# Performance work log

Measured on AMD Instinct MI355X. Metric: run time of the kernel, lower is better.

The kernel has to match this reference:

```python
import jax, jax.numpy as jnp
import numpy as np

B, H, W = 8, 64, 64
DIM, NH, WS = 384, 6, 14
HD = DIM // NH
MLP = int(DIM * 4.0)
EPS = 1e-5
SCALE = HD ** -0.5


def setup_inputs() -> dict:
    key = jax.random.key(0)
    ks = jax.random.split(key, 8)
    init = lambda k, shape: (jax.random.normal(k, shape, dtype=jnp.float32) * 0.02)
    return {
        "x": jax.random.normal(ks[0], (B, H, W, DIM), dtype=jnp.float32),
        "ln1_w": jnp.ones((DIM,), jnp.float32),
        "ln1_b": jnp.zeros((DIM,), jnp.float32),
        "qkv_w": init(ks[1], (DIM, 3 * DIM)),
        "qkv_b": jnp.zeros((3 * DIM,), jnp.float32),
        "proj_w": init(ks[2], (DIM, DIM)),
        "proj_b": jnp.zeros((DIM,), jnp.float32),
        "rel_pos_h": init(ks[3], (2 * WS - 1, HD)),
        "rel_pos_w": init(ks[4], (2 * WS - 1, HD)),
        "ln2_w": jnp.ones((DIM,), jnp.float32),
        "ln2_b": jnp.zeros((DIM,), jnp.float32),
        "fc1_w": init(ks[5], (DIM, MLP)),
        "fc1_b": jnp.zeros((MLP,), jnp.float32),
        "fc2_w": init(ks[6], (MLP, DIM)),
        "fc2_b": jnp.zeros((DIM,), jnp.float32),
    }


def _layernorm(x, w, b):
    m = x.mean(-1, keepdims=True)
    v = ((x - m) ** 2).mean(-1, keepdims=True)
    return (x - m) * jax.lax.rsqrt(v + EPS) * w + b


def _get_rel_pos(rel_pos, ws):
    # q_size == k_size == ws and rel_pos has 2*ws-1 rows, so torch's
    # F.interpolate to max_rel_dist=2*ws-1 is an identity; direct indexing.
    coords = jnp.arange(ws)[:, None] - jnp.arange(ws)[None, :] + (ws - 1)
    return rel_pos[coords]  # (ws, ws, head_dim)


def _attention(xw, qkv_w, qkv_b, proj_w, proj_b, rel_pos_h, rel_pos_w):
    Bw = xw.shape[0]
    N = WS * WS
    qkv = xw.reshape(Bw, N, DIM) @ qkv_w + qkv_b  # (Bw, N, 3*DIM)
    qkv = qkv.reshape(Bw, N, 3, NH, HD).transpose(2, 0, 3, 1, 4).reshape(3, Bw * NH, N, HD)
    q, k, v = qkv[0], qkv[1], qkv[2]
    attn = jnp.einsum("bqd,bkd->bqk", q * SCALE, k)  # (Bw*NH, N, N)
    Rh = _get_rel_pos(rel_pos_h, WS)
    Rw = _get_rel_pos(rel_pos_w, WS)
    rq = q.reshape(Bw * NH, WS, WS, HD)
    rel_h = jnp.einsum("bhwc,hkc->bhwk", rq, Rh)
    rel_w = jnp.einsum("bhwc,wkc->bhwk", rq, Rw)
    attn = (attn.reshape(Bw * NH, WS, WS, WS, WS)
            + rel_h[:, :, :, :, None]
            + rel_w[:, :, :, None, :]).reshape(Bw * NH, N, N)
    attn = jax.nn.softmax(attn, axis=-1)
    out = jnp.einsum("bqk,bkd->bqd", attn, v)
    out = out.reshape(Bw, NH, WS, WS, HD).transpose(0, 2, 3, 1, 4).reshape(Bw, WS, WS, DIM)
    return out @ proj_w + proj_b


def reference(x, ln1_w, ln1_b, qkv_w, qkv_b, proj_w, proj_b, rel_pos_h, rel_pos_w,
              ln2_w, ln2_b, fc1_w, fc1_b, fc2_w, fc2_b):
    shortcut = x
    h = _layernorm(x, ln1_w, ln1_b)
    pad_h = (WS - H % WS) % WS
    pad_w = (WS - W % WS) % WS
    Hp, Wp = H + pad_h, W + pad_w
    hp = jnp.pad(h, ((0, 0), (0, pad_h), (0, pad_w), (0, 0)))
    # window partition: (B, Hp, Wp, C) -> (B*nWin, WS, WS, C)
    wins = hp.reshape(B, Hp // WS, WS, Wp // WS, WS, DIM)
    wins = wins.transpose(0, 1, 3, 2, 4, 5).reshape(-1, WS, WS, DIM)
    wins = _attention(wins, qkv_w, qkv_b, proj_w, proj_b, rel_pos_h, rel_pos_w)
    # window unpartition
    y = wins.reshape(B, Hp // WS, Wp // WS, WS, WS, DIM)
    y = y.transpose(0, 1, 3, 2, 4, 5).reshape(B, Hp, Wp, DIM)[:, :H, :W, :]
    x = shortcut + y
    h2 = _layernorm(x, ln2_w, ln2_b)
    mlp = jax.nn.gelu(h2 @ fc1_w + fc1_b, approximate=False) @ fc2_w + fc2_b
    return x + mlp
```

## Files before the change

kernel.cpp:

```cpp
#include <hip/hip_runtime.h>
#include <math.h>

#define DIMC 384
#define NHD  6
#define HD   64
#define WSZ  14
#define NTOK 196
#define NWIN 200
#define NWH  1200
#define MWIN 39200
#define MX   32768
#define MLPD 1536

typedef short short8 __attribute__((ext_vector_type(8)));
typedef float f32x4 __attribute__((ext_vector_type(4)));
typedef float f32x16 __attribute__((ext_vector_type(16)));

__device__ __forceinline__ unsigned short f2bf(float f) {
  unsigned int u = __float_as_uint(f);
  u = (u + 0x7fffu + ((u >> 16) & 1u)) >> 16;
  return (unsigned short)u;
}
__device__ __forceinline__ unsigned int pkbf(float a, float b) {
  unsigned int r; asm("v_cvt_pk_bf16_f32 %0, %1, %2" : "=v"(r) : "v"(a), "v"(b)); return r;
}
__device__ __forceinline__ float gelu_t(float x) {
  float z = 1.5957691216057308f * (x + 0.044715f * x * x * x);
  float e = __expf(z);
  float th = 1.f - 2.f * __builtin_amdgcn_rcpf(e + 1.f);
  return 0.5f * x * (1.f + th);
}

typedef const __attribute__((address_space(1))) unsigned int* gptr_t;
typedef __attribute__((address_space(3))) unsigned int* lptr_t;
__device__ __forceinline__ void gload16(const unsigned short* g, unsigned short* l) {
  __builtin_amdgcn_global_load_lds((gptr_t)(const void*)g, (lptr_t)(void*)l, 16, 0, 0);
}

#define SEG0 442368
#define SEG1 589824
#define SEG2 1179648
#define SEG3 1769472
#define SEG4 1773568
#define SEG5 2003968
__global__ void prep_kernel(const float* __restrict__ qkvw, const float* __restrict__ projw,
                            const float* __restrict__ fc1w, const float* __restrict__ fc2w,
                            const float* __restrict__ relh, const float* __restrict__ relw,
                            unsigned short* __restrict__ qkvwT, unsigned short* __restrict__ projwT,
                            unsigned short* __restrict__ fc1wT, unsigned short* __restrict__ fc2wT,
                            unsigned short* __restrict__ relcat, unsigned short* __restrict__ vT) {
  int id = blockIdx.x * 256 + threadIdx.x;
  if (id < SEG0) {
    int n = id / 384, k = id - n * 384;
    qkvwT[id] = f2bf(qkvw[(size_t)k * 1152 + n]);
  } else if (id < SEG1) {
    id -= SEG0;
    int n = id / 384, k = id - n * 384;
    projwT[id] = f2bf(projw[(size_t)k * 384 + n]);
  } else if (id < SEG2) {
    id -= SEG1;
    int n = id / 384, k = id - n * 384;
    fc1wT[id] = f2bf(fc1w[(size_t)k * 1536 + n]);
  } else if (id < SEG3) {
    id -= SEG2;
    int n = id / 1536, k = id - n * 1536;
    fc2wT[id] = f2bf(fc2w[(size_t)k * 384 + n]);
  } else if (id < SEG4) {
    id -= SEG3;
    int rc = id >> 6, d = id & 63;
    float v = 0.f;
    if (rc < 27) v = relh[rc * 64 + d] * 8.f;
    else if (rc < 54) v = relw[(rc - 27) * 64 + d] * 8.f;
    relcat[id] = f2bf(v);
  } else if (id < SEG5) {
    id -= SEG4;
    int row = id / 3, part = id - row * 3;
    *(int2*)(vT + (size_t)row * 208 + 196 + part * 4) = make_int2(0, 0);
  }
}

__global__ __launch_bounds__(64) void ln1win_kernel(const float* __restrict__ x,
    const float* __restrict__ w, const float* __restrict__ b, unsigned short* __restrict__ xw) {
  int t = blockIdx.x;
  int lane = threadIdx.x;
  int win = t / NTOK, p = t - win * NTOK;
  int bb = win / 25, rem = win - bb * 25;
  int wi = rem / 5, wj = rem - wi * 5;
  int i = p / WSZ, j = p - i * WSZ;
  int r = wi * WSZ + i, c = wj * WSZ + j;
  unsigned short* o = xw + (size_t)t * DIMC;
  if (r >= 64 || c >= 64) {
    #pragma unroll
    for (int q = 0; q < 6; q++) o[lane + q * 64] = 0;
    return;
  }
  const float* xr = x + (((size_t)bb * 64 + r) * 64 + c) * DIMC;
  float v[6]; float s = 0.f, s2 = 0.f;
  #pragma unroll
  for (int q = 0; q < 6; q++) { float f = xr[lane + q * 64]; v[q] = f; s += f; s2 += f * f; }
  #pragma unroll
  for (int off = 32; off; off >>= 1) { s += __shfl_xor(s, off); s2 += __shfl_xor(s2, off); }
  float mean = s * (1.f / DIMC);
  float var  = s2 * (1.f / DIMC) - mean * mean;
  float rstd = rsqrtf(var + 1e-5f);
  #pragma unroll
  for (int q = 0; q < 6; q++) {
    int d = lane + q * 64;
    o[d] = f2bf((v[q] - mean) * rstd * w[d] + b[d]);
  }
}

__global__ __launch_bounds__(64) void ln2_kernel(const float* __restrict__ x2,
    const float* __restrict__ w, const float* __restrict__ b, unsigned short* __restrict__ h2) {
  int t = blockIdx.x; int lane = threadIdx.x;
  const float* xr = x2 + (size_t)t * DIMC;
  unsigned short* o = h2 + (size_t)t * DIMC;
  float v[6]; float s = 0.f, s2 = 0.f;
  #pragma unroll
  for (int q = 0; q < 6; q++) { float f = xr[lane + q * 64]; v[q] = f; s += f; s2 += f * f; }
  #pragma unroll
  for (int off = 32; off; off >>= 1) { s += __shfl_xor(s, off); s2 += __shfl_xor(s2, off); }
  float mean = s * (1.f / DIMC);
  float var  = s2 * (1.f / DIMC) - mean * mean;
  float rstd = rsqrtf(var + 1e-5f);
  #pragma unroll
  for (int q = 0; q < 6; q++) {
    int d = lane + q * 64;
    o[d] = f2bf((v[q] - mean) * rstd * w[d] + b[d]);
  }
}

template <int EPI>
__global__ __launch_bounds__(256) void gemm_kernel(
    const unsigned short* __restrict__ A, const unsigned short* __restrict__ WT,
    int Mrows, int Kd,
    const float* __restrict__ bias, const float* __restrict__ addin,
    float* __restrict__ outf, unsigned short* __restrict__ outb,
    unsigned short* __restrict__ outb2) {
  __shared__ unsigned short As[3][128 * 32];
  __shared__ unsigned short Bs[3][128 * 32];
  const int nwg = gridDim.x * gridDim.y;
  const int flat = blockIdx.y * gridDim.x + blockIdx.x;
  const int xcd = flat & 7, q_ = nwg >> 3, r_ = nwg & 7;
  const int wg = (xcd < r_ ? xcd * (q_ + 1) : r_ * (q_ + 1) + (xcd - r_) * q_) + (flat >> 3);
  const int bx = wg / gridDim.y, by = wg - bx * gridDim.y;
  const int row0 = bx * 128, col0 = by * 128;
  const int tid = threadIdx.x;
  const int l = tid & 63, wid = tid >> 6;
  const int fr = l & 15, fk = (l >> 4) * 8;
  const int wr = (wid >> 1) * 64, wc = (wid & 1) * 64;
  const int sr = l >> 2, sc = (l & 3) * 8;
  const int scs = sc ^ (((sr >> 1) & 3) << 3);
  const int rsw = ((fr >> 1) & 3) << 3;
  f32x4 acc[4][4] = {};
  const unsigned short* ap = A + (size_t)row0 * Kd;
  const unsigned short* bp = WT + (size_t)col0 * Kd;
  const int nt = Kd >> 5;

  auto stage = [&](int t, int b) {
    const int k0 = t * 32;
    #pragma unroll
    for (int j = 0; j < 2; j++) {
      int chunk = j * 4 + wid;
      gload16(ap + (size_t)(chunk * 16 + sr) * Kd + k0 + scs, &As[b][chunk * 512]);
      gload16(bp + (size_t)(chunk * 16 + sr) * Kd + k0 + scs, &Bs[b][chunk * 512]);
    }
  };
  stage(0, 0);
  stage(1, 1);
  int c = 0;
  for (int t = 0; t < nt; ++t) {
    if (t < nt - 1) asm volatile("s_waitcnt vmcnt(4)" ::: "memory");
    else            asm volatile("s_waitcnt vmcnt(0)" ::: "memory");
    __builtin_amdgcn_s_barrier();
    __builtin_amdgcn_sched_barrier(0);
    if (t + 2 < nt) stage(t + 2, (c + 2 >= 3) ? c - 1 : c + 2);
    short8 a[4], b[4];
    #pragma unroll
    for (int fi = 0; fi < 4; fi++) {
      a[fi] = *(const short8*)&As[c][(wr + fi * 16 + fr) * 32 + (fk ^ rsw)];
      b[fi] = *(const short8*)&Bs[c][(wc + fi * 16 + fr) * 32 + (fk ^ rsw)];
    }
    __builtin_amdgcn_s_setprio(1);
    #pragma unroll
    for (int fi = 0; fi < 4; fi++)
      #pragma unroll
      for (int fj = 0; fj < 4; fj++)
        acc[fi][fj] = __builtin_amdgcn_mfma_f32_16x16x32_bf16(b[fj], a[fi], acc[fi][fj], 0, 0, 0);
    __builtin_amdgcn_s_setprio(0);
    c = (c + 1 >= 3) ? 0 : c + 1;
  }
  #pragma unroll
  for (int fi = 0; fi < 4; fi++) {
    const int gr = row0 + wr + fi * 16 + fr;
    if (gr >= Mrows) continue;
    int wv_ = 0, p = 0, valid = 1; size_t pixbase = 0;
    if (EPI == 0 || EPI == 1) { wv_ = gr / NTOK; p = gr - wv_ * NTOK; }
    if (EPI == 1) {
      int bb = wv_ / 25, rem2 = wv_ - bb * 25;
      int wi = rem2 / 5, wj = rem2 - wi * 5;
      int i = p / WSZ, j = p - i * WSZ;
      int rr = wi * WSZ + i, cc = wj * WSZ + j;
      valid = (rr < 64) && (cc < 64);
      pixbase = (((size_t)bb * 64 + rr) * 64 + cc) * DIMC;
    }
    #pragma unroll
    for (int fj = 0; fj < 4; fj++) {
      const int gcb = col0 + wc + fj * 16 + (l >> 4) * 4;
      f32x4 v = acc[fi][fj];
      float4 bv = *(const float4*)&bias[gcb];
      float t0 = v[0] + bv.x, t1 = v[1] + bv.y, t2 = v[2] + bv.z, t3 = v[3] + bv.w;
      if (EPI == 0) {
        int s = gcb / 384, rem = gcb - s * 384;
        int hh = rem >> 6, d0 = gcb & 63;
        int whh = wv_ * NHD + hh;
        if (s == 0) { t0 *= 0.125f; t1 *= 0.125f; t2 *= 0.125f; t3 *= 0.125f; }
        if (s < 2) {
          *(int2*)&outb[((size_t)s * NWH + whh) * (NTOK * 64) + p * 64 + d0] =
              make_int2((int)pkbf(t0, t1), (int)pkbf(t2, t3));
        } else {
          unsigned short* vb = outb2 + ((size_t)whh * 64 + d0) * 208 + p;
          vb[0] = f2bf(t0); vb[208] = f2bf(t1); vb[416] = f2bf(t2); vb[624] = f2bf(t3);
        }
      } else if (EPI == 1) {
        if (valid) {
          size_t idx = pixbase + gcb;
          float4 ad = *(const float4*)&addin[idx];
          *(float4*)&outf[idx] = make_float4(t0 + ad.x, t1 + ad.y, t2 + ad.z, t3 + ad.w);
        }
      } else if (EPI == 2) {
        *(int2*)&outb[(size_t)gr * MLPD + gcb] =
            make_int2((int)pkbf(gelu_t(t0), gelu_t(t1)), (int)pkbf(gelu_t(t2), gelu_t(t3)));
      } else {
        size_t idx = (size_t)gr * DIMC + gcb;
        float4 ad = *(const float4*)&addin[idx];
        *(float4*)&outf[idx] = make_float4(t0 + ad.x, t1 + ad.y, t2 + ad.z, t3 + ad.w);
      }
    }
  }
}

template <bool TAIL>
__device__ __forceinline__ void attn_chunk(
    int kk, int l31, int hi,
    const unsigned short* __restrict__ kg,
    const unsigned short* __restrict__ VT,
    const short8* qf, const short8* qrel,
    f32x16& olo, f32x16& ohi_, float& m_reg, float& s_run) {
  int key = kk * 32 + l31;
  int keyc = (TAIL && key > 195) ? 195 : key;
  f32x16 S = {};
  __builtin_amdgcn_s_setprio(1);
  #pragma unroll
  for (int m = 0; m < 4; m++) {
    short8 kf = *(const short8*)(kg + (size_t)keyc * 64 + m * 16 + hi * 8);
    S = __builtin_amdgcn_mfma_f32_32x32x16_bf16(kf, qf[m], S, 0, 0, 0);
  }
  {
    int ki = keyc / 14, kj = keyc - ki * 14;
    #pragma unroll
    for (int m2 = 0; m2 < 2; m2++) {
      short8 kh;
      #pragma unroll
      for (int j = 0; j < 8; j++) {
        int cc = m2 * 16 + hi * 8 + j;
        kh[j] = (short)((cc == ki || cc == 14 + kj) ? 0x3F80 : 0);
      }
      S = __builtin_amdgcn_mfma_f32_32x32x16_bf16(kh, qrel[m2], S, 0, 0, 0);
    }
  }
  __builtin_amdgcn_s_setprio(0);
  float pmax = -3e38f;
  #pragma unroll
  for (int r = 0; r < 16; r++) {
    if (TAIL) {
      int krow = kk * 32 + (r & 3) + 8 * (r >> 2) + 4 * hi;
      if (krow >= 196) S[r] = -3e38f;
    }
    pmax = fmaxf(pmax, S[r]);
  }
  pmax = fmaxf(pmax, __shfl_xor(pmax, 32));
  if (__any(pmax > m_reg + 8.f)) {
    float m_new = fmaxf(m_reg, pmax);
    float fac = __expf(m_reg - m_new);
    m_reg = m_new;
    s_run *= fac;
    #pragma unroll
    for (int r = 0; r < 16; r++) {
      int qr = (r & 3) + 8 * (r >> 2) + 4 * hi;
      float fr_ = __shfl(fac, qr);
      olo[r] *= fr_; ohi_[r] *= fr_;
    }
  }
  float psum = 0.f;
  #pragma unroll
  for (int r = 0; r < 16; r++) { S[r] = __expf(S[r] - m_reg); psum += S[r]; }
  s_run += psum;
  unsigned int pk[8];
  #pragma unroll
  for (int t = 0; t < 8; t++) pk[t] = pkbf(S[2 * t], S[2 * t + 1]);
  #pragma unroll
  for (int m2 = 0; m2 < 2; m2++) {
    int b_ = m2 * 4;
    unsigned int x0 = (unsigned int)__shfl_xor((int)pk[b_ + 0], 32);
    unsigned int x1 = (unsigned int)__shfl_xor((int)pk[b_ + 1], 32);
    unsigned int x2 = (unsigned int)__shfl_xor((int)pk[b_ + 2], 32);
    unsigned int x3 = (unsigned int)__shfl_xor((int)pk[b_ + 3], 32);
    unsigned int au[4];
    au[0] = hi ? x2 : pk[b_ + 0];
    au[1] = hi ? x3 : pk[b_ + 1];
    au[2] = hi ? pk[b_ + 2] : x0;
    au[3] = hi ? pk[b_ + 3] : x1;
    short8 pa; __builtin_memcpy(&pa, au, 16);
    int kb = kk * 32 + m2 * 16 + hi * 8;
    if (TAIL && kb > 208) kb = 208;
    short8 vblo = *(const short8*)&VT[l31 * 216 + kb];
    short8 vbhi = *(const short8*)&VT[(32 + l31) * 216 + kb];
    __builtin_amdgcn_s_setprio(1);
    olo  = __builtin_amdgcn_mfma_f32_32x32x16_bf16(pa, vblo, olo, 0, 0, 0);
    ohi_ = __builtin_amdgcn_mfma_f32_32x32x16_bf16(pa, vbhi, ohi_, 0, 0, 0);
    __builtin_amdgcn_s_setprio(0);
  }
}

__global__ __launch_bounds__(256) void attn32_kernel(
    const unsigned short* __restrict__ qk_g,
    const unsigned short* __restrict__ vT_g,
    const unsigned short* __restrict__ relcat,
    unsigned short* __restrict__ attnout) {
  __shared__ __align__(16) unsigned short VT[64 * 216];
  __shared__ __align__(16) unsigned short RELB[4][2048];
  const int wh = blockIdx.x, y = blockIdx.y;
  const int w = wh / NHD, h = wh - w * NHD;
  const int tid = threadIdx.x;
  const unsigned short* vrow = vT_g + (size_t)wh * 64 * 208;
  for (int e = tid; e < 64 * 27; e += 256) {
    int d = e / 27, c = e - d * 27;
    int4 val = {0, 0, 0, 0};
    if (c < 26) val = *(const int4*)(vrow + d * 208 + c * 8);
    *(int4*)&VT[d * 216 + c * 8] = val;
  }
  __syncthreads();
  const int l = tid & 63, wv = tid >> 6;
  const int l31 = l & 31, hi = l >> 5;
  unsigned short* RB = &RELB[wv][0];
  const unsigned short* qg = qk_g + (size_t)wh * (NTOK * 64);
  const unsigned short* kg = qk_g + (size_t)(NWH + wh) * (NTOK * 64);

  const int tbeg = y ? 4 : 0, tend = y ? 7 : 4;
  for (int tile = tbeg + wv; tile < tend; tile += 4) {
    const int q0 = tile * 32;
    int qrow = q0 + l31; if (qrow > 195) qrow = 195;
    short8 qf[4];
    #pragma unroll
    for (int m = 0; m < 4; m++)
      qf[m] = *(const short8*)(qg + (size_t)qrow * 64 + m * 16 + hi * 8);
    #pragma unroll
    for (int rt = 0; rt < 2; rt++) {
      f32x16 cr = {};
      __builtin_amdgcn_s_setprio(1);
      #pragma unroll
      for (int m = 0; m < 4; m++) {
        short8 af = *(const short8*)(relcat + (rt * 32 + l31) * 64 + m * 16 + hi * 8);
        cr = __builtin_amdgcn_mfma_f32_32x32x16_bf16(af, qf[m], cr, 0, 0, 0);
      }
      __builtin_amdgcn_s_setprio(0);
      #pragma unroll
      for (int t = 0; t < 8; t++) {
        int rr = rt * 32 + ((2 * t) & 3) + 8 * (t >> 1) + 4 * hi;
        *(unsigned int*)&RB[l31 * 64 + rr] = pkbf(cr[2 * t], cr[2 * t + 1]);
      }
    }
    __builtin_amdgcn_wave_barrier();
    int qi = qrow / 14, qj = qrow - qi * 14;
    short8 qrel[2];
    #pragma unroll
    for (int m2 = 0; m2 < 2; m2++)
      #pragma unroll
      for (int j = 0; j < 8; j++) {
        int cc = m2 * 16 + hi * 8 + j;
        unsigned short vv = 0;
        if (cc < 14) vv = RB[l31 * 64 + (qi - cc + 13)];
        else if (cc < 28) vv = RB[l31 * 64 + 27 + (qj - (cc - 14) + 13)];
        qrel[m2][j] = (short)vv;
      }
    __builtin_amdgcn_wave_barrier();
    f32x16 olo = {}, ohi_ = {};
    float m_reg = -3e38f, s_run = 0.f;
    for (int kk = 0; kk < 6; kk++)
      attn_chunk<false>(kk, l31, hi, kg, VT, qf, qrel, olo, ohi_, m_reg, s_run);
    attn_chunk<true>(6, l31, hi, kg, VT, qf, qrel, olo, ohi_, m_reg, s_run);
    s_run += __shfl_xor(s_run, 32);
    float inv = 1.f / s_run;
    #pragma unroll
    for (int r = 0; r < 16; r++) {
      int qr = (r & 3) + 8 * (r >> 2) + 4 * hi;
      float ir = __shfl(inv, qr);
      int tok = q0 + qr;
      if (tok < 196) {
        size_t base = ((size_t)w * NTOK + tok) * DIMC + h * 64;
        attnout[base + l31] = f2bf(olo[r] * ir);
        attnout[base + 32 + l31] = f2bf(ohi_[r] * ir);
      }
    }
  }
}

extern "C" void kernel_launch(void* const* d_in, const int* in_sizes, int n_in,
                              void* d_out, int out_size, void* d_ws, size_t ws_size,
                              hipStream_t stream) {
  const float* x     = (const float*)d_in[0];
  const float* ln1w  = (const float*)d_in[1];
  const float* ln1b  = (const float*)d_in[2];
  const float* qkvw  = (const float*)d_in[3];
  const float* qkvb  = (const float*)d_in[4];
  const float* projw = (const float*)d_in[5];
  const float* projb = (const float*)d_in[6];
  const float* relh  = (const float*)d_in[7];
  const float* relw  = (const float*)d_in[8];
  const float* ln2w  = (const float*)d_in[9];
  const float* ln2b  = (const float*)d_in[10];
  const float* fc1w  = (const float*)d_in[11];
  const float* fc1b  = (const float*)d_in[12];
  const float* fc2w  = (const float*)d_in[13];
  const float* fc2b  = (const float*)d_in[14];

  const size_t R0 = 0;
  const size_t R1 = R0 + 50331648;
  const size_t R2 = R1 + 100663296;
  const size_t R3 = R2 + 30408704;
  const size_t NEED = R3 + 3547136;
  if (ws_size < NEED) return;
  char* ws = (char*)d_ws;
  unsigned short* xw     = (unsigned short*)(ws + R0);
  float*          x2     = (float*)(ws + R0);
  unsigned short* qk_g   = (unsigned short*)(ws + R1);
  unsigned short* vT_g   = qk_g + (size_t)2 * NWH * NTOK * 64;
  unsigned short* hidden = (unsigned short*)(ws + R1);
  unsigned short* attno  = (unsigned short*)(ws + R2);
  unsigned short* h2     = (unsigned short*)(ws + R2);
  unsigned short* qkvwT  = (unsigned short*)(ws + R3);
  unsigned short* projwT = qkvwT + 442368;
  unsigned short* fc1wT  = projwT + 147456;
  unsigned short* fc2wT  = fc1wT + 589824;
  unsigned short* relcat = fc2wT + 589824;

  prep_kernel<<<7829, 256, 0, stream>>>(qkvw, projw, fc1w, fc2w, relh, relw,
                                        qkvwT, projwT, fc1wT, fc2wT, relcat, vT_g);
  ln1win_kernel<<<MWIN, 64, 0, stream>>>(x, ln1w, ln1b, xw);
  gemm_kernel<0><<<dim3(307, 9), 256, 0, stream>>>(xw, qkvwT, MWIN, 384, qkvb, nullptr, nullptr, qk_g, vT_g);
  attn32_kernel<<<dim3(NWH, 2), 256, 0, stream>>>(qk_g, vT_g, relcat, attno);
  gemm_kernel<1><<<dim3(307, 3), 256, 0, stream>>>(attno, projwT, MWIN, 384, projb, x, x2, nullptr, nullptr);
  ln2_kernel<<<MX, 64, 0, stream>>>(x2, ln2w, ln2b, h2);
  gemm_kernel<2><<<dim3(256, 12), 256, 0, stream>>>(h2, fc1wT, MX, 384, fc1b, nullptr, nullptr, hidden, nullptr);
  gemm_kernel<3><<<dim3(256, 3), 256, 0, stream>>>(hidden, fc2wT, MX, 1536, fc2b, x2, (float*)d_out, nullptr, nullptr);
}
```

Before: 349.7 us.

## Store residual x2 in bf16, merge LN1 into prep kernel, widen LN blocks

The post-attention residual x2 is now written as bf16 instead of fp32, which halves its write traffic and its reads in LN2 and in the fc2 residual epilogue. The LN1 window-partition kernel is folded into the weight-prep kernel so one launch does both. Both layernorms now run four rows per 256-thread block instead of one row per 64-thread block. Keeping the residual in bf16 loses precision in the skip path, which could affect accuracy against the fp32 reference.

```diff
diff --git a/kernel.cpp b/kernel.cpp
--- a/kernel.cpp
+++ b/kernel.cpp
@@ -21,6 +21,9 @@
   u = (u + 0x7fffu + ((u >> 16) & 1u)) >> 16;
   return (unsigned short)u;
 }
+__device__ __forceinline__ float bf2f(unsigned int u) {
+  return __uint_as_float(u << 16);
+}
 __device__ __forceinline__ unsigned int pkbf(float a, float b) {
   unsigned int r; asm("v_cvt_pk_bf16_f32 %0, %1, %2" : "=v"(r) : "v"(a), "v"(b)); return r;
 }
@@ -37,19 +40,54 @@
   __builtin_amdgcn_global_load_lds((gptr_t)(const void*)g, (lptr_t)(void*)l, 16, 0, 0);
 }
 
+#define LN1BLKS 9800
 #define SEG0 442368
 #define SEG1 589824
 #define SEG2 1179648
 #define SEG3 1769472
 #define SEG4 1773568
 #define SEG5 2003968
-__global__ void prep_kernel(const float* __restrict__ qkvw, const float* __restrict__ projw,
-                            const float* __restrict__ fc1w, const float* __restrict__ fc2w,
-                            const float* __restrict__ relh, const float* __restrict__ relw,
-                            unsigned short* __restrict__ qkvwT, unsigned short* __restrict__ projwT,
-                            unsigned short* __restrict__ fc1wT, unsigned short* __restrict__ fc2wT,
-                            unsigned short* __restrict__ relcat, unsigned short* __restrict__ vT) {
-  int id = blockIdx.x * 256 + threadIdx.x;
+__global__ __launch_bounds__(256) void pre_kernel(
+    const float* __restrict__ x, const float* __restrict__ ln1w, const float* __restrict__ ln1b,
+    const float* __restrict__ qkvw, const float* __restrict__ projw,
+    const float* __restrict__ fc1w, const float* __restrict__ fc2w,
+    const float* __restrict__ relh, const float* __restrict__ relw,
+    unsigned short* __restrict__ xw,
+    unsigned short* __restrict__ qkvwT, unsigned short* __restrict__ projwT,
+    unsigned short* __restrict__ fc1wT, unsigned short* __restrict__ fc2wT,
+    unsigned short* __restrict__ relcat, unsigned short* __restrict__ vT) {
+  const int blk = blockIdx.x;
+  if (blk < LN1BLKS) {
+    int t = blk * 4 + (threadIdx.x >> 6);
+    int lane = threadIdx.x & 63;
+    int win = t / NTOK, p = t - win * NTOK;
+    int bb = win / 25, rem = win - bb * 25;
+    int wi = rem / 5, wj = rem - wi * 5;
+    int i = p / WSZ, j = p - i * WSZ;
+    int r = wi * WSZ + i, c = wj * WSZ + j;
+    unsigned short* o = xw + (size_t)t * DIMC;
+    if (r >= 64 || c >= 64) {
+      #pragma unroll
+      for (int q = 0; q < 6; q++) o[lane + q * 64] = 0;
+      return;
+    }
+    const float* xr = x + (((size_t)bb * 64 + r) * 64 + c) * DIMC;
+    float v[6]; float s = 0.f, s2 = 0.f;
+    #pragma unroll
+    for (int q = 0; q < 6; q++) { float f = xr[lane + q * 64]; v[q] = f; s += f; s2 += f * f; }
+    #pragma unroll
+    for (int off = 32; off; off >>= 1) { s += __shfl_xor(s, off); s2 += __shfl_xor(s2, off); }
+    float mean = s * (1.f / DIMC);
+    float var  = s2 * (1.f / DIMC) - mean * mean;
+    float rstd = rsqrtf(var + 1e-5f);
+    #pragma unroll
+    for (int q = 0; q < 6; q++) {
+      int d = lane + q * 64;
+      o[d] = f2bf((v[q] - mean) * rstd * ln1w[d] + ln1b[d]);
+    }
+    return;
+  }
+  int id = (blk - LN1BLKS) * 256 + threadIdx.x;
   if (id < SEG0) {
     int n = id / 384, k = id - n * 384;
     qkvwT[id] = f2bf(qkvw[(size_t)k * 1152 + n]);
@@ -79,25 +117,15 @@
   }
 }
 
-__global__ __launch_bounds__(64) void ln1win_kernel(const float* __restrict__ x,
-    const float* __restrict__ w, const float* __restrict__ b, unsigned short* __restrict__ xw) {
-  int t = blockIdx.x;
-  int lane = threadIdx.x;
-  int win = t / NTOK, p = t - win * NTOK;
-  int bb = win / 25, rem = win - bb * 25;
-  int wi = rem / 5, wj = rem - wi * 5;
-  int i = p / WSZ, j = p - i * WSZ;
-  int r = wi * WSZ + i, c = wj * WSZ + j;
-  unsigned short* o = xw + (size_t)t * DIMC;
-  if (r >= 64 || c >= 64) {
-    #pragma unroll
-    for (int q = 0; q < 6; q++) o[lane + q * 64] = 0;
-    return;
-  }
-  const float* xr = x + (((size_t)bb * 64 + r) * 64 + c) * DIMC;
+__global__ __launch_bounds__(256) void ln2_kernel(const unsigned short* __restrict__ x2b,
+    const float* __restrict__ w, const float* __restrict__ b, unsigned short* __restrict__ h2) {
+  int t = blockIdx.x * 4 + (threadIdx.x >> 6);
+  int lane = threadIdx.x & 63;
+  const unsigned short* xr = x2b + (size_t)t * DIMC;
+  unsigned short* o = h2 + (size_t)t * DIMC;
   float v[6]; float s = 0.f, s2 = 0.f;
   #pragma unroll
-  for (int q = 0; q < 6; q++) { float f = xr[lane + q * 64]; v[q] = f; s += f; s2 += f * f; }
+  for (int q = 0; q < 6; q++) { float f = bf2f(xr[lane + q * 64]); v[q] = f; s += f; s2 += f * f; }
   #pragma unroll
   for (int off = 32; off; off >>= 1) { s += __shfl_xor(s, off); s2 += __shfl_xor(s2, off); }
   float mean = s * (1.f / DIMC);
@@ -110,31 +138,12 @@
   }
 }
 
-__global__ __launch_bounds__(64) void ln2_kernel(const float* __restrict__ x2,
-    const float* __restrict__ w, const float* __restrict__ b, unsigned short* __restrict__ h2) {
-  int t = blockIdx.x; int lane = threadIdx.x;
-  const float* xr = x2 + (size_t)t * DIMC;
-  unsigned short* o = h2 + (size_t)t * DIMC;
-  float v[6]; float s = 0.f, s2 = 0.f;
-  #pragma unroll
-  for (int q = 0; q < 6; q++) { float f = xr[lane + q * 64]; v[q] = f; s += f; s2 += f * f; }
-  #pragma unroll
-  for (int off = 32; off; off >>= 1) { s += __shfl_xor(s, off); s2 += __shfl_xor(s2, off); }
-  float mean = s * (1.f / DIMC);
-  float var  = s2 * (1.f / DIMC) - mean * mean;
-  float rstd = rsqrtf(var + 1e-5f);
-  #pragma unroll
-  for (int q = 0; q < 6; q++) {
-    int d = lane + q * 64;
-    o[d] = f2bf((v[q] - mean) * rstd * w[d] + b[d]);
-  }
-}
-
 template <int EPI>
 __global__ __launch_bounds__(256) void gemm_kernel(
     const unsigned short* __restrict__ A, const unsigned short* __restrict__ WT,
     int Mrows, int Kd,
-    const float* __restrict__ bias, const float* __restrict__ addin,
+    const float* __restrict__ bias,
+    const float* __restrict__ addinf, const unsigned short* __restrict__ addinb,
     float* __restrict__ outf, unsigned short* __restrict__ outb,
     unsigned short* __restrict__ outb2) {
   __shared__ unsigned short As[3][128 * 32];
@@ -225,16 +234,20 @@
       } else if (EPI == 1) {
         if (valid) {
           size_t idx = pixbase + gcb;
-          float4 ad = *(const float4*)&addin[idx];
-          *(float4*)&outf[idx] = make_float4(t0 + ad.x, t1 + ad.y, t2 + ad.z, t3 + ad.w);
+          float4 ad = *(const float4*)&addinf[idx];
+          *(int2*)&outb[idx] = make_int2((int)pkbf(t0 + ad.x, t1 + ad.y),
+                                         (int)pkbf(t2 + ad.z, t3 + ad.w));
         }
       } else if (EPI == 2) {
         *(int2*)&outb[(size_t)gr * MLPD + gcb] =
             make_int2((int)pkbf(gelu_t(t0), gelu_t(t1)), (int)pkbf(gelu_t(t2), gelu_t(t3)));
       } else {
         size_t idx = (size_t)gr * DIMC + gcb;
-        float4 ad = *(const float4*)&addin[idx];
-        *(float4*)&outf[idx] = make_float4(t0 + ad.x, t1 + ad.y, t2 + ad.z, t3 + ad.w);
+        int2 adp = *(const int2*)&addinb[idx];
+        unsigned int u0 = (unsigned int)adp.x, u1 = (unsigned int)adp.y;
+        float4 o = make_float4(t0 + bf2f(u0 & 0xffffu), t1 + bf2f(u0 >> 16),
+                               t2 + bf2f(u1 & 0xffffu), t3 + bf2f(u1 >> 16));
+        *(float4*)&outf[idx] = o;
       }
     }
   }
@@ -433,7 +446,7 @@
   if (ws_size < NEED) return;
   char* ws = (char*)d_ws;
   unsigned short* xw     = (unsigned short*)(ws + R0);
-  float*          x2     = (float*)(ws + R0);
+  unsigned short* x2b    = (unsigned short*)(ws + R0);
   unsigned short* qk_g   = (unsigned short*)(ws + R1);
   unsigned short* vT_g   = qk_g + (size_t)2 * NWH * NTOK * 64;
   unsigned short* hidden = (unsigned short*)(ws + R1);
@@ -445,13 +458,17 @@
   unsigned short* fc2wT  = fc1wT + 589824;
   unsigned short* relcat = fc2wT + 589824;
 
-  prep_kernel<<<7829, 256, 0, stream>>>(qkvw, projw, fc1w, fc2w, relh, relw,
-                                        qkvwT, projwT, fc1wT, fc2wT, relcat, vT_g);
-  ln1win_kernel<<<MWIN, 64, 0, stream>>>(x, ln1w, ln1b, xw);
-  gemm_kernel<0><<<dim3(307, 9), 256, 0, stream>>>(xw, qkvwT, MWIN, 384, qkvb, nullptr, nullptr, qk_g, vT_g);
+  pre_kernel<<<LN1BLKS + 7828, 256, 0, stream>>>(x, ln1w, ln1b, qkvw, projw, fc1w, fc2w,
+                                                 relh, relw, xw, qkvwT, projwT, fc1wT,
+                                                 fc2wT, relcat, vT_g);
+  gemm_kernel<0><<<dim3(307, 9), 256, 0, stream>>>(xw, qkvwT, MWIN, 384, qkvb,
+                                                   nullptr, nullptr, nullptr, qk_g, vT_g);
   attn32_kernel<<<dim3(NWH, 2), 256, 0, stream>>>(qk_g, vT_g, relcat, attno);
-  gemm_kernel<1><<<dim3(307, 3), 256, 0, stream>>>(attno, projwT, MWIN, 384, projb, x, x2, nullptr, nullptr);
-  ln2_kernel<<<MX, 64, 0, stream>>>(x2, ln2w, ln2b, h2);
-  gemm_kernel<2><<<dim3(256, 12), 256, 0, stream>>>(h2, fc1wT, MX, 384, fc1b, nullptr, nullptr, hidden, nullptr);
-  gemm_kernel<3><<<dim3(256, 3), 256, 0, stream>>>(hidden, fc2wT, MX, 1536, fc2b, x2, (float*)d_out, nullptr, nullptr);
-}
+  gemm_kernel<1><<<dim3(307, 3), 256, 0, stream>>>(attno, projwT, MWIN, 384, projb,
+                                                   x, nullptr, nullptr, x2b, nullptr);
+  ln2_kernel<<<8192, 256, 0, stream>>>(x2b, ln2w, ln2b, h2);
+  gemm_kernel<2><<<dim3(256, 12), 256, 0, stream>>>(h2, fc1wT, MX, 384, fc1b,
+                                                    nullptr, nullptr, nullptr, hidden, nullptr);
+  gemm_kernel<3><<<dim3(256, 3), 256, 0, stream>>>(hidden, fc2wT, MX, 1536, fc2b,
+                                                   nullptr, x2b, (float*)d_out, nullptr, nullptr);
+}
```

After: 340.5 us (median of 2 runs). 2.6% less time.
